# Kernel tuning notes

Hardware: AMD Instinct MI355X
Metric: run time of the kernel (lower is better)

## Reference

```python
import jax, jax.numpy as jnp
from jax import lax
import numpy as np

B, T, H, E = 4096, 16, 1024, 1024


def setup_inputs() -> dict:
    key = jax.random.key(0)
    ks = jax.random.split(key, 6)
    query = jax.random.normal(ks[0], (B, H), dtype=jnp.float32)
    topics = jax.random.normal(ks[1], (B, T, E), dtype=jnp.float32)
    coverage_vector = jax.random.uniform(ks[2], (B, T), dtype=jnp.float32)
    # Ua: Linear(embed->hidden, bias=False); weight [H, E]
    Ua_w = jax.random.normal(ks[3], (H, E), dtype=jnp.float32) * 0.03
    # Wa: Linear(hidden->hidden, bias=False). Applied repeatedly (T times) to
    # query in the original loop, so keep spectral norm < 1 for stability.
    Wa_w = jax.random.normal(ks[4], (H, H), dtype=jnp.float32) * 0.01
    # va: Linear(hidden->1, bias=True)
    va_w = jax.random.normal(ks[5], (1, H), dtype=jnp.float32) * 0.03
    va_b = jnp.zeros((1,), dtype=jnp.float32)
    return {"query": query, "topics": topics, "coverage_vector": coverage_vector,
            "Ua_w": Ua_w, "Wa_w": Wa_w, "va_w": va_w, "va_b": va_b}


def reference(query, topics, coverage_vector, Ua_w, Wa_w, va_w, va_b):
    # proj_key for all steps at once: Ua(topics[:, i, :]) -> [B, T, H]
    proj_keys = jnp.einsum('bte,he->bth', topics, Ua_w)
    # Original loop mutates query = Wa(query) each step, so step i uses
    # Wa^(i+1) @ query. Sequential dependence -> lax.scan over T.
    def step(q, pk_c):
        pk, c = pk_c                       # pk: [B, H], c: [B]
        q = q @ Wa_w.T                     # query = Wa(query)
        s = (jnp.tanh(q + pk) @ va_w.T)[:, 0] + va_b[0]  # va(tanh(.)) -> [B]
        return q, s * c                    # scale by coverage C_t[:, i]
    xs = (jnp.swapaxes(proj_keys, 0, 1), coverage_vector.T)  # [T,B,H], [T,B]
    _, scores = lax.scan(step, query, xs)  # scores: [T, B]
    scores = scores.T                      # [B, T]
    alphas = jax.nn.softmax(scores, axis=1)
    mt = jnp.einsum('bt,bte->be', alphas, topics)  # bmm(alphas[:,None,:], topics)
    return mt, alphas
```

## Files before the change

### kernel.cpp

```cpp
#include <hip/hip_runtime.h>

typedef unsigned short u16;
typedef unsigned int u32;
typedef __attribute__((ext_vector_type(8))) __bf16 bf16x8;
typedef __attribute__((ext_vector_type(4))) float f32x4;

__device__ __forceinline__ u16 f2bf(float f) {
  u32 u = __float_as_uint(f);
  u32 r = (u + 0x7FFFu + ((u >> 16) & 1u)) >> 16;
  return (u16)r;
}

__device__ __forceinline__ void gload_lds16(const void* g, void* l) {
  __builtin_amdgcn_global_load_lds((const __attribute__((address_space(1))) u32*)g,
                                   (__attribute__((address_space(3))) u32*)l, 16, 0, 0);
}

__device__ __forceinline__ float fast_tanh(float x) {
  x = fminf(fmaxf(x, -15.f), 15.f);
  float e2 = __expf(2.f * x);
  return (e2 - 1.f) / (e2 + 1.f);
}

__global__ __launch_bounds__(256) void cvt_kernel(const float* __restrict__ src,
                                                  u16* __restrict__ dst, int n4) {
  int stride = gridDim.x * blockDim.x;
  for (int i = blockIdx.x * blockDim.x + threadIdx.x; i < n4; i += stride) {
    float4 v = reinterpret_cast<const float4*>(src)[i];
    ushort4 o;
    o.x = f2bf(v.x); o.y = f2bf(v.y); o.z = f2bf(v.z); o.w = f2bf(v.w);
    reinterpret_cast<ushort4*>(dst)[i] = o;
  }
}

__global__ __launch_bounds__(256) void cvt3_kernel(const float* __restrict__ q_src, u16* __restrict__ q_dst,
                                                   const float* __restrict__ u_src, u16* __restrict__ u_dst,
                                                   const float* __restrict__ w_src, u16* __restrict__ w_dst) {
  int b = blockIdx.x;
  const float* src; u16* dst; int i;
  if (b < 4096)      { src = q_src; dst = q_dst; i = b * 256 + threadIdx.x; }
  else if (b < 5120) { src = u_src; dst = u_dst; i = (b - 4096) * 256 + threadIdx.x; }
  else               { src = w_src; dst = w_dst; i = (b - 5120) * 256 + threadIdx.x; }
  float4 v = reinterpret_cast<const float4*>(src)[i];
  ushort4 o;
  o.x = f2bf(v.x); o.y = f2bf(v.y); o.z = f2bf(v.z); o.w = f2bf(v.w);
  reinterpret_cast<ushort4*>(dst)[i] = o;
}

__global__ __launch_bounds__(256) void transpose_bf16_kernel(const float* __restrict__ src,
                                                             u16* __restrict__ dst) {
  __shared__ float tile[32][33];
  int tx = threadIdx.x & 31, ty = threadIdx.x >> 5;
  int bx = blockIdx.x * 32, by = blockIdx.y * 32;
#pragma unroll
  for (int j = 0; j < 32; j += 8)
    tile[ty + j][tx] = src[(size_t)(by + ty + j) * 1024 + bx + tx];
  __syncthreads();
#pragma unroll
  for (int j = 0; j < 32; j += 8)
    dst[(size_t)(bx + ty + j) * 1024 + by + tx] = f2bf(tile[tx][ty + j]);
}

__device__ __forceinline__ void stage_tile(const u16* __restrict__ g, size_t row_stride,
                                           u16* lds, int tid) {
#pragma unroll
  for (int s = 0; s < 4; ++s) {
    int chunk = s * 256 + tid;
    int row = chunk >> 3;
    int kcl = (chunk & 7) ^ (row & 7);
    const u16* gp = g + (size_t)row * row_stride + (size_t)(kcl * 8);
    u16* lp = lds + (tid >> 6) * 512 + s * 2048;
    gload_lds16(gp, lp);
  }
}

struct PowArgs {
  const u16* A[8];
  const u16* Bt[8];
  u16* C[8];
  u16* Ct[8];
};

__global__ __launch_bounds__(256) void pow_gemm_kernel(PowArgs args) {
  const u16* A  = args.A[blockIdx.z];
  const u16* Bt = args.Bt[blockIdx.z];
  u16* C  = args.C[blockIdx.z];
  u16* Ct = args.Ct[blockIdx.z];

  __shared__ __align__(16) u16 As[8192];
  __shared__ __align__(16) u16 Bs[8192];

  int tid = threadIdx.x;
  int lane = tid & 63, wave = tid >> 6;
  int wr = wave >> 1, wc = wave & 1;
  int lr = lane & 15, lg = lane >> 4;
  int m0 = blockIdx.x * 128, n0 = blockIdx.y * 128;

  f32x4 acc[4][4];
  const f32x4 zero = {0.f, 0.f, 0.f, 0.f};
#pragma unroll
  for (int m = 0; m < 4; ++m)
#pragma unroll
    for (int n = 0; n < 4; ++n) acc[m][n] = zero;

  for (int k0 = 0; k0 < 1024; k0 += 64) {
    stage_tile(A + (size_t)m0 * 1024 + k0, 1024, As, tid);
    stage_tile(Bt + (size_t)n0 * 1024 + k0, 1024, Bs, tid);
    __syncthreads();
#pragma unroll
    for (int ks = 0; ks < 2; ++ks) {
      bf16x8 a[4], b[4];
#pragma unroll
      for (int m = 0; m < 4; ++m) {
        int ra = wr * 64 + m * 16 + lr;
        a[m] = *reinterpret_cast<const bf16x8*>(As + ra * 64 + (((ks * 4 + lg) ^ (ra & 7)) << 3));
      }
#pragma unroll
      for (int n = 0; n < 4; ++n) {
        int rb = wc * 64 + n * 16 + lr;
        b[n] = *reinterpret_cast<const bf16x8*>(Bs + rb * 64 + (((ks * 4 + lg) ^ (rb & 7)) << 3));
      }
#pragma unroll
      for (int m = 0; m < 4; ++m)
#pragma unroll
        for (int n = 0; n < 4; ++n)
          acc[m][n] = __builtin_amdgcn_mfma_f32_16x16x32_bf16(a[m], b[n], acc[m][n], 0, 0, 0);
    }
    __syncthreads();
  }

#pragma unroll
  for (int m = 0; m < 4; ++m) {
    int row0 = m0 + wr * 64 + m * 16 + lg * 4;
#pragma unroll
    for (int n = 0; n < 4; ++n) {
      int col = n0 + wc * 64 + n * 16 + lr;
      f32x4 c = acc[m][n];
      ushort4 pk;
      pk.x = f2bf(c[0]); pk.y = f2bf(c[1]); pk.z = f2bf(c[2]); pk.w = f2bf(c[3]);
      C[(size_t)(row0 + 0) * 1024 + col] = pk.x;
      C[(size_t)(row0 + 1) * 1024 + col] = pk.y;
      C[(size_t)(row0 + 2) * 1024 + col] = pk.z;
      C[(size_t)(row0 + 3) * 1024 + col] = pk.w;
      *reinterpret_cast<ushort4*>(Ct + (size_t)col * 1024 + row0) = pk;
    }
  }
}


#define PHASE_READS(CUR, KS, MH)                                                 \
  { _Pragma("unroll") for (int i_ = 0; i_ < 4; ++i_) af[i_] = lda(CUR, KS, (MH)*4 + i_); \
    if ((MH) == 0) { _Pragma("unroll") for (int n_ = 0; n_ < 4; ++n_) bfr[n_] = ldb(CUR, KS, n_); } }

#define PHASE_MFMA(MH)                                                           \
  { __builtin_amdgcn_s_barrier();                                                \
    asm volatile("s_waitcnt lgkmcnt(0)" ::: "memory");                           \
    __builtin_amdgcn_sched_barrier(0);                                           \
    __builtin_amdgcn_s_setprio(1);                                               \
    _Pragma("unroll") for (int i_ = 0; i_ < 4; ++i_)                             \
      _Pragma("unroll") for (int n_ = 0; n_ < 4; ++n_)                           \
        acc[(MH)*4 + i_][n_] =                                                   \
            __builtin_amdgcn_mfma_f32_16x16x32_bf16(af[i_], bfr[n_], acc[(MH)*4 + i_][n_], 0, 0, 0); \
    __builtin_amdgcn_s_setprio(0); }

#define PHASE_END()                                                              \
  { __builtin_amdgcn_s_barrier(); __builtin_amdgcn_sched_barrier(0); }

__global__ __launch_bounds__(512, 2) void score8_kernel(
    const u16* __restrict__ query_bf, const u16* __restrict__ topics_bf,
    const u16* __restrict__ F_base, const u16* __restrict__ Ua_bf,
    const float* __restrict__ va_w, float* __restrict__ scores_raw) {
  extern __shared__ __align__(16) char lds[];

  const int tid = threadIdx.x;
  const int lane = tid & 63, wave = tid >> 6;
  const int wm = wave >> 2, wn = wave & 3;
  const int lr = lane & 15, lg = lane >> 4;
  const int m0 = blockIdx.x * 256, n0 = blockIdx.y * 256;
  const int t = blockIdx.z;
  const int NT = 32;

  const u16* Ft = F_base + (size_t)t * (1024 * 1024);

  auto a_src = [&](int kt, const u16*& p, int& str) {
    if (kt < 16) { p = query_bf + (size_t)m0 * 1024 + kt * 64; str = 1024; }
    else { p = topics_bf + (size_t)m0 * 16384 + (size_t)t * 1024 + (kt - 16) * 64; str = 16384; }
  };
  auto b_src = [&](int kt, const u16*& p, int& str) {
    if (kt < 16) { p = Ft + (size_t)n0 * 1024 + kt * 64; str = 1024; }
    else { p = Ua_bf + (size_t)n0 * 1024 + (kt - 16) * 64; str = 1024; }
  };

  auto stage = [&](const u16* p, int str, int ks, int lds_byte) {
#pragma unroll
    for (int s = 0; s < 2; ++s) {
      int c = s * 512 + tid;
      int row = c >> 2;
      int cl = (c & 3) ^ ((row >> 1) & 3);
      const u16* gp = p + (size_t)row * str + ks * 32 + cl * 8;
      char* lp = lds + lds_byte + s * 8192 + (tid >> 6) * 1024;
      gload_lds16(gp, lp);
    }
  };

  auto lda = [&](int cur, int ks, int m) -> bf16x8 {
    int row = wm * 128 + m * 16 + lr;
    int byte = cur * 65536 + ks * 16384 + row * 64 + ((lg ^ ((row >> 1) & 3)) << 4);
    return *reinterpret_cast<const bf16x8*>(lds + byte);
  };
  auto ldb = [&](int cur, int ks, int n) -> bf16x8 {
    int row = wn * 64 + n * 16 + lr;
    int byte = cur * 65536 + 32768 + ks * 16384 + row * 64 + ((lg ^ ((row >> 1) & 3)) << 4);
    return *reinterpret_cast<const bf16x8*>(lds + byte);
  };

  f32x4 acc[8][4];
  const f32x4 zero = {0.f, 0.f, 0.f, 0.f};
#pragma unroll
  for (int m = 0; m < 8; ++m)
#pragma unroll
    for (int n = 0; n < 4; ++n) acc[m][n] = zero;

  bf16x8 af[4], bfr[4];
  const u16 *ap, *bp; int as_, bs_;

  a_src(0, ap, as_); stage(ap, as_, 0, 0);
  b_src(0, bp, bs_); stage(bp, bs_, 0, 32768);
  a_src(0, ap, as_); stage(ap, as_, 1, 16384);
  b_src(0, bp, bs_); stage(bp, bs_, 1, 49152);
  a_src(1, ap, as_); stage(ap, as_, 0, 65536);
  b_src(1, bp, bs_); stage(bp, bs_, 0, 65536 + 32768);
  asm volatile("s_waitcnt vmcnt(4)" ::: "memory");
  __builtin_amdgcn_s_barrier();
  __builtin_amdgcn_sched_barrier(0);

#pragma unroll 2
  for (int kt = 0; kt < NT; ++kt) {
    int cur = kt & 1, nxt = cur ^ 1;
    PHASE_READS(cur, 0, 0);
    if (kt + 1 < NT) { a_src(kt + 1, ap, as_); stage(ap, as_, 1, nxt * 65536 + 16384); }
    PHASE_MFMA(0); PHASE_END();
    PHASE_READS(cur, 0, 1);
    if (kt + 1 < NT) { b_src(kt + 1, bp, bs_); stage(bp, bs_, 1, nxt * 65536 + 49152); }
    PHASE_MFMA(1); PHASE_END();
    PHASE_READS(cur, 1, 0);
    if (kt + 2 < NT) { a_src(kt + 2, ap, as_); stage(ap, as_, 0, cur * 65536); }
    PHASE_MFMA(0); PHASE_END();
    PHASE_READS(cur, 1, 1);
    if (kt + 2 < NT) { b_src(kt + 2, bp, bs_); stage(bp, bs_, 0, cur * 65536 + 32768); }
    PHASE_MFMA(1);
    if (kt < NT - 2)       { asm volatile("s_waitcnt vmcnt(4)" ::: "memory"); }
    else if (kt == NT - 2) { asm volatile("s_waitcnt vmcnt(0)" ::: "memory"); }
    PHASE_END();
  }

  float va_c[4];
#pragma unroll
  for (int n = 0; n < 4; ++n) va_c[n] = va_w[n0 + wn * 64 + n * 16 + lr];

  float* sred = (float*)lds;
#pragma unroll
  for (int m = 0; m < 8; ++m) {
    float rs[4] = {0.f, 0.f, 0.f, 0.f};
#pragma unroll
    for (int n = 0; n < 4; ++n) {
      f32x4 c = acc[m][n];
      rs[0] += va_c[n] * fast_tanh(c[0]);
      rs[1] += va_c[n] * fast_tanh(c[1]);
      rs[2] += va_c[n] * fast_tanh(c[2]);
      rs[3] += va_c[n] * fast_tanh(c[3]);
    }
#pragma unroll
    for (int j = 0; j < 4; ++j) {
      float v = rs[j];
      v += __shfl_xor(v, 1);
      v += __shfl_xor(v, 2);
      v += __shfl_xor(v, 4);
      v += __shfl_xor(v, 8);
      if (lr == 0) sred[wn * 256 + wm * 128 + m * 16 + lg * 4 + j] = v;
    }
  }
  __syncthreads();
  if (tid < 256) {
    float s = sred[tid] + sred[256 + tid] + sred[512 + tid] + sred[768 + tid];
    atomicAdd(&scores_raw[(size_t)(m0 + tid) * 16 + t], s);
  }
}

__global__ __launch_bounds__(256) void softmax_mt_kernel(
    const float* __restrict__ scores_raw, const float* __restrict__ cov,
    const float* __restrict__ topics, const float* __restrict__ va_b,
    float* __restrict__ mt, float* __restrict__ alphas) {
  int b = blockIdx.x;
  int tid = threadIdx.x;
  float vb = va_b[0];
  float e[16];
  float mx = -3.4e38f;
#pragma unroll
  for (int t = 0; t < 16; ++t) {
    float s = (scores_raw[b * 16 + t] + vb) * cov[b * 16 + t];
    e[t] = s;
    mx = fmaxf(mx, s);
  }
  float sum = 0.f;
#pragma unroll
  for (int t = 0; t < 16; ++t) { e[t] = __expf(e[t] - mx); sum += e[t]; }
  float inv = 1.f / sum;
  if (tid == 0) {
#pragma unroll
    for (int t = 0; t < 16; ++t) alphas[b * 16 + t] = e[t] * inv;
  }
  const float4* tp = reinterpret_cast<const float4*>(topics + (size_t)b * 16384);
  float4 accv = {0.f, 0.f, 0.f, 0.f};
#pragma unroll
  for (int t = 0; t < 16; ++t) {
    float4 v = tp[t * 256 + tid];
    float a = e[t] * inv;
    accv.x += a * v.x; accv.y += a * v.y; accv.z += a * v.z; accv.w += a * v.w;
  }
  reinterpret_cast<float4*>(mt + (size_t)b * 1024)[tid] = accv;
}

extern "C" void kernel_launch(void* const* d_in, const int* in_sizes, int n_in,
                              void* d_out, int out_size, void* d_ws, size_t ws_size,
                              hipStream_t stream) {
  (void)in_sizes; (void)n_in; (void)out_size; (void)ws_size;
  const float* query = (const float*)d_in[0];
  const float* topics = (const float*)d_in[1];
  const float* cov   = (const float*)d_in[2];
  const float* Ua    = (const float*)d_in[3];
  const float* Wa    = (const float*)d_in[4];
  const float* va_w  = (const float*)d_in[5];
  const float* va_b  = (const float*)d_in[6];

  float* mt = (float*)d_out;
  float* alphas = mt + (size_t)4096 * 1024;

  char* ws = (char*)d_ws;
  u16* topics_bf = (u16*)(ws);
  u16* query_bf  = (u16*)(ws + (size_t)128 * 1024 * 1024);
  u16* Ua_bf     = (u16*)(ws + (size_t)136 * 1024 * 1024);
  u16* F_base    = (u16*)(ws + (size_t)138 * 1024 * 1024);
  u16* FT_base   = (u16*)(ws + (size_t)170 * 1024 * 1024);
  float* scores_raw = (float*)(ws + (size_t)202 * 1024 * 1024);

  hipFuncSetAttribute(reinterpret_cast<const void*>(score8_kernel),
                      hipFuncAttributeMaxDynamicSharedMemorySize, 131072);

  hipMemsetAsync(scores_raw, 0, (size_t)4096 * 16 * sizeof(float), stream);

  cvt_kernel<<<8192, 256, 0, stream>>>(topics, topics_bf, 16777216);
  cvt3_kernel<<<6144, 256, 0, stream>>>(query, query_bf, Ua, Ua_bf, Wa, F_base);
  transpose_bf16_kernel<<<dim3(32, 32), 256, 0, stream>>>(Wa, FT_base);

  const size_t MS = 1024 * 1024;
  auto F  = [&](int i) { return F_base + (size_t)i * MS; };
  auto FT = [&](int i) { return FT_base + (size_t)i * MS; };

  PowArgs a1{};
  a1.A[0] = F(0); a1.Bt[0] = FT(0); a1.C[0] = F(1); a1.Ct[0] = FT(1);
  pow_gemm_kernel<<<dim3(8, 8, 1), 256, 0, stream>>>(a1);
  PowArgs a2{};
  a2.A[0] = F(1); a2.Bt[0] = FT(0); a2.C[0] = F(2); a2.Ct[0] = FT(2);
  a2.A[1] = F(1); a2.Bt[1] = FT(1); a2.C[1] = F(3); a2.Ct[1] = FT(3);
  pow_gemm_kernel<<<dim3(8, 8, 2), 256, 0, stream>>>(a2);
  PowArgs a3{};
  for (int p = 0; p < 4; ++p) { a3.A[p] = F(3); a3.Bt[p] = FT(p); a3.C[p] = F(4 + p); a3.Ct[p] = FT(4 + p); }
  pow_gemm_kernel<<<dim3(8, 8, 4), 256, 0, stream>>>(a3);
  PowArgs a4{};
  for (int p = 0; p < 8; ++p) { a4.A[p] = F(7); a4.Bt[p] = FT(p); a4.C[p] = F(8 + p); a4.Ct[p] = FT(8 + p); }
  pow_gemm_kernel<<<dim3(8, 8, 8), 256, 0, stream>>>(a4);

  score8_kernel<<<dim3(16, 4, 16), 512, 131072, stream>>>(query_bf, topics_bf, F_base, Ua_bf,
                                                          va_w, scores_raw);
  softmax_mt_kernel<<<4096, 256, 0, stream>>>(scores_raw, cov, topics, va_b, mt, alphas);
}
```

Before: 823.0 us.

## Use 64x64-tile GEMM for early Wa powers and precompute score kernel offsets

Adds a smaller-tile pow64_gemm kernel for the first two Wa power stages, which had too few 128x128 blocks to fill the GPU. It also rearranges the score kernel's LDS layout into separate A/B regions and precomputes per-lane LDS and global offsets, removing per-iteration address arithmetic and branchy source selection. The small-tile kernel has no double buffering and gets less reuse, and the precomputed offsets add register pressure.

```diff
diff --git a/kernel.cpp b/kernel.cpp
--- a/kernel.cpp
+++ b/kernel.cpp
@@ -147,23 +147,105 @@
   }
 }
 
-
-#define PHASE_READS(CUR, KS, MH)                                                 \
-  { _Pragma("unroll") for (int i_ = 0; i_ < 4; ++i_) af[i_] = lda(CUR, KS, (MH)*4 + i_); \
-    if ((MH) == 0) { _Pragma("unroll") for (int n_ = 0; n_ < 4; ++n_) bfr[n_] = ldb(CUR, KS, n_); } }
-
-#define PHASE_MFMA(MH)                                                           \
-  { __builtin_amdgcn_s_barrier();                                                \
-    asm volatile("s_waitcnt lgkmcnt(0)" ::: "memory");                           \
-    __builtin_amdgcn_sched_barrier(0);                                           \
-    __builtin_amdgcn_s_setprio(1);                                               \
-    _Pragma("unroll") for (int i_ = 0; i_ < 4; ++i_)                             \
-      _Pragma("unroll") for (int n_ = 0; n_ < 4; ++n_)                           \
-        acc[(MH)*4 + i_][n_] =                                                   \
+__device__ __forceinline__ void stage_tile64(const u16* __restrict__ g, u16* lds, int tid) {
+#pragma unroll
+  for (int s = 0; s < 2; ++s) {
+    int chunk = s * 256 + tid;
+    int row = chunk >> 3;
+    int kcl = (chunk & 7) ^ (row & 7);
+    const u16* gp = g + (size_t)row * 1024 + (size_t)(kcl * 8);
+    u16* lp = lds + (tid >> 6) * 512 + s * 2048;
+    gload_lds16(gp, lp);
+  }
+}
+
+__global__ __launch_bounds__(256) void pow64_gemm_kernel(PowArgs args) {
+  const u16* A  = args.A[blockIdx.z];
+  const u16* Bt = args.Bt[blockIdx.z];
+  u16* C  = args.C[blockIdx.z];
+  u16* Ct = args.Ct[blockIdx.z];
+
+  __shared__ __align__(16) u16 As[4096];
+  __shared__ __align__(16) u16 Bs[4096];
+
+  int tid = threadIdx.x;
+  int lane = tid & 63, wave = tid >> 6;
+  int wr = wave >> 1, wc = wave & 1;
+  int lr = lane & 15, lg = lane >> 4;
+  int m0 = blockIdx.x * 64, n0 = blockIdx.y * 64;
+
+  f32x4 acc[2][2];
+  const f32x4 zero = {0.f, 0.f, 0.f, 0.f};
+#pragma unroll
+  for (int m = 0; m < 2; ++m)
+#pragma unroll
+    for (int n = 0; n < 2; ++n) acc[m][n] = zero;
+
+  for (int k0 = 0; k0 < 1024; k0 += 64) {
+    stage_tile64(A + (size_t)m0 * 1024 + k0, As, tid);
+    stage_tile64(Bt + (size_t)n0 * 1024 + k0, Bs, tid);
+    __syncthreads();
+#pragma unroll
+    for (int ks = 0; ks < 2; ++ks) {
+      bf16x8 a[2], b[2];
+#pragma unroll
+      for (int m = 0; m < 2; ++m) {
+        int ra = wr * 32 + m * 16 + lr;
+        a[m] = *reinterpret_cast<const bf16x8*>(As + ra * 64 + (((ks * 4 + lg) ^ (ra & 7)) << 3));
+      }
+#pragma unroll
+      for (int n = 0; n < 2; ++n) {
+        int rb = wc * 32 + n * 16 + lr;
+        b[n] = *reinterpret_cast<const bf16x8*>(Bs + rb * 64 + (((ks * 4 + lg) ^ (rb & 7)) << 3));
+      }
+#pragma unroll
+      for (int m = 0; m < 2; ++m)
+#pragma unroll
+        for (int n = 0; n < 2; ++n)
+          acc[m][n] = __builtin_amdgcn_mfma_f32_16x16x32_bf16(a[m], b[n], acc[m][n], 0, 0, 0);
+    }
+    __syncthreads();
+  }
+
+#pragma unroll
+  for (int m = 0; m < 2; ++m) {
+    int row0 = m0 + wr * 32 + m * 16 + lg * 4;
+#pragma unroll
+    for (int n = 0; n < 2; ++n) {
+      int col = n0 + wc * 32 + n * 16 + lr;
+      f32x4 c = acc[m][n];
+      ushort4 pk;
+      pk.x = f2bf(c[0]); pk.y = f2bf(c[1]); pk.z = f2bf(c[2]); pk.w = f2bf(c[3]);
+      C[(size_t)(row0 + 0) * 1024 + col] = pk.x;
+      C[(size_t)(row0 + 1) * 1024 + col] = pk.y;
+      C[(size_t)(row0 + 2) * 1024 + col] = pk.z;
+      C[(size_t)(row0 + 3) * 1024 + col] = pk.w;
+      *reinterpret_cast<ushort4*>(Ct + (size_t)col * 1024 + row0) = pk;
+    }
+  }
+}
+
+
+#define PHASE_READS(CUR, KS, MH)                                                     \
+  { _Pragma("unroll") for (int i_ = 0; i_ < 4; ++i_)                                 \
+      af[i_] = *reinterpret_cast<const bf16x8*>(lds + aoffv[(MH)*4 + i_] +           \
+                                                (CUR)*32768 + (KS)*16384);           \
+    if ((MH) == 0) { _Pragma("unroll") for (int n_ = 0; n_ < 4; ++n_)                \
+      bfr[n_] = *reinterpret_cast<const bf16x8*>(lds + boffv[n_] +                   \
+                                                 (CUR)*32768 + (KS)*16384); } }
+
+#define PHASE_MFMA(MH)                                                               \
+  { __builtin_amdgcn_s_barrier();                                                    \
+    asm volatile("s_waitcnt lgkmcnt(0)" ::: "memory");                               \
+    __builtin_amdgcn_sched_barrier(0);                                               \
+    __builtin_amdgcn_s_setprio(1);                                                   \
+    _Pragma("unroll") for (int i_ = 0; i_ < 4; ++i_)                                 \
+      _Pragma("unroll") for (int n_ = 0; n_ < 4; ++n_)                               \
+        acc[(MH)*4 + i_][n_] =                                                       \
             __builtin_amdgcn_mfma_f32_16x16x32_bf16(af[i_], bfr[n_], acc[(MH)*4 + i_][n_], 0, 0, 0); \
     __builtin_amdgcn_s_setprio(0); }
 
-#define PHASE_END()                                                              \
+#define PHASE_END()                                                                  \
   { __builtin_amdgcn_s_barrier(); __builtin_amdgcn_sched_barrier(0); }
 
 __global__ __launch_bounds__(512, 2) void score8_kernel(
@@ -182,36 +264,46 @@
 
   const u16* Ft = F_base + (size_t)t * (1024 * 1024);
 
-  auto a_src = [&](int kt, const u16*& p, int& str) {
-    if (kt < 16) { p = query_bf + (size_t)m0 * 1024 + kt * 64; str = 1024; }
-    else { p = topics_bf + (size_t)m0 * 16384 + (size_t)t * 1024 + (kt - 16) * 64; str = 16384; }
+  u32 aoffv[8], boffv[4];
+#pragma unroll
+  for (int m = 0; m < 8; ++m) {
+    int row = wm * 128 + m * 16 + lr;
+    aoffv[m] = row * 64 + ((lg ^ ((row >> 1) & 3)) << 4);
+  }
+#pragma unroll
+  for (int n = 0; n < 4; ++n) {
+    int row = wn * 64 + n * 16 + lr;
+    boffv[n] = 65536 + row * 64 + ((lg ^ ((row >> 1) & 3)) << 4);
+  }
+
+  u32 goff1[2], goff2[2];
+#pragma unroll
+  for (int s = 0; s < 2; ++s) {
+    int c = s * 512 + tid;
+    int row = c >> 2;
+    int cl = (c & 3) ^ ((row >> 1) & 3);
+    goff1[s] = row * 1024 + cl * 8;
+    goff2[s] = row * 16384 + cl * 8;
+  }
+  char* sdst = lds + (tid >> 6) * 1024;
+  const u16* qbase = query_bf + (size_t)m0 * 1024;
+  const u16* tbase = topics_bf + (size_t)m0 * 16384 + (size_t)t * 1024 - 1024;
+  const u16* fbase = Ft + (size_t)n0 * 1024;
+  const u16* ubase = Ua_bf + (size_t)n0 * 1024 - 1024;
+
+  auto stageA = [&](int kt, int ks, int buf) {
+    const u16* base = (kt < 16 ? qbase : tbase) + kt * 64 + ks * 32;
+#pragma unroll
+    for (int s = 0; s < 2; ++s) {
+      u32 off = (kt < 16) ? goff1[s] : goff2[s];
+      gload_lds16(base + off, sdst + buf * 32768 + ks * 16384 + s * 8192);
+    }
   };
-  auto b_src = [&](int kt, const u16*& p, int& str) {
-    if (kt < 16) { p = Ft + (size_t)n0 * 1024 + kt * 64; str = 1024; }
-    else { p = Ua_bf + (size_t)n0 * 1024 + (kt - 16) * 64; str = 1024; }
-  };
-
-  auto stage = [&](const u16* p, int str, int ks, int lds_byte) {
-#pragma unroll
-    for (int s = 0; s < 2; ++s) {
-      int c = s * 512 + tid;
-      int row = c >> 2;
-      int cl = (c & 3) ^ ((row >> 1) & 3);
-      const u16* gp = p + (size_t)row * str + ks * 32 + cl * 8;
-      char* lp = lds + lds_byte + s * 8192 + (tid >> 6) * 1024;
-      gload_lds16(gp, lp);
-    }
-  };
-
-  auto lda = [&](int cur, int ks, int m) -> bf16x8 {
-    int row = wm * 128 + m * 16 + lr;
-    int byte = cur * 65536 + ks * 16384 + row * 64 + ((lg ^ ((row >> 1) & 3)) << 4);
-    return *reinterpret_cast<const bf16x8*>(lds + byte);
-  };
-  auto ldb = [&](int cur, int ks, int n) -> bf16x8 {
-    int row = wn * 64 + n * 16 + lr;
-    int byte = cur * 65536 + 32768 + ks * 16384 + row * 64 + ((lg ^ ((row >> 1) & 3)) << 4);
-    return *reinterpret_cast<const bf16x8*>(lds + byte);
+  auto stageB = [&](int kt, int ks, int buf) {
+    const u16* base = (kt < 16 ? fbase : ubase) + kt * 64 + ks * 32;
+#pragma unroll
+    for (int s = 0; s < 2; ++s)
+      gload_lds16(base + goff1[s], sdst + 65536 + buf * 32768 + ks * 16384 + s * 8192);
   };
 
   f32x4 acc[8][4];
@@ -222,14 +314,10 @@
     for (int n = 0; n < 4; ++n) acc[m][n] = zero;
 
   bf16x8 af[4], bfr[4];
-  const u16 *ap, *bp; int as_, bs_;
-
-  a_src(0, ap, as_); stage(ap, as_, 0, 0);
-  b_src(0, bp, bs_); stage(bp, bs_, 0, 32768);
-  a_src(0, ap, as_); stage(ap, as_, 1, 16384);
-  b_src(0, bp, bs_); stage(bp, bs_, 1, 49152);
-  a_src(1, ap, as_); stage(ap, as_, 0, 65536);
-  b_src(1, bp, bs_); stage(bp, bs_, 0, 65536 + 32768);
+
+  stageA(0, 0, 0); stageB(0, 0, 0);
+  stageA(0, 1, 0); stageB(0, 1, 0);
+  stageA(1, 0, 1); stageB(1, 0, 1);
   asm volatile("s_waitcnt vmcnt(4)" ::: "memory");
   __builtin_amdgcn_s_barrier();
   __builtin_amdgcn_sched_barrier(0);
@@ -238,16 +326,16 @@
   for (int kt = 0; kt < NT; ++kt) {
     int cur = kt & 1, nxt = cur ^ 1;
     PHASE_READS(cur, 0, 0);
-    if (kt + 1 < NT) { a_src(kt + 1, ap, as_); stage(ap, as_, 1, nxt * 65536 + 16384); }
+    if (kt + 1 < NT) stageA(kt + 1, 1, nxt);
     PHASE_MFMA(0); PHASE_END();
     PHASE_READS(cur, 0, 1);
-    if (kt + 1 < NT) { b_src(kt + 1, bp, bs_); stage(bp, bs_, 1, nxt * 65536 + 49152); }
+    if (kt + 1 < NT) stageB(kt + 1, 1, nxt);
     PHASE_MFMA(1); PHASE_END();
     PHASE_READS(cur, 1, 0);
-    if (kt + 2 < NT) { a_src(kt + 2, ap, as_); stage(ap, as_, 0, cur * 65536); }
+    if (kt + 2 < NT) stageA(kt + 2, 0, cur);
     PHASE_MFMA(0); PHASE_END();
     PHASE_READS(cur, 1, 1);
-    if (kt + 2 < NT) { b_src(kt + 2, bp, bs_); stage(bp, bs_, 0, cur * 65536 + 32768); }
+    if (kt + 2 < NT) stageB(kt + 2, 0, cur);
     PHASE_MFMA(1);
     if (kt < NT - 2)       { asm volatile("s_waitcnt vmcnt(4)" ::: "memory"); }
     else if (kt == NT - 2) { asm volatile("s_waitcnt vmcnt(0)" ::: "memory"); }
@@ -359,11 +447,11 @@
 
   PowArgs a1{};
   a1.A[0] = F(0); a1.Bt[0] = FT(0); a1.C[0] = F(1); a1.Ct[0] = FT(1);
-  pow_gemm_kernel<<<dim3(8, 8, 1), 256, 0, stream>>>(a1);
+  pow64_gemm_kernel<<<dim3(16, 16, 1), 256, 0, stream>>>(a1);
   PowArgs a2{};
   a2.A[0] = F(1); a2.Bt[0] = FT(0); a2.C[0] = F(2); a2.Ct[0] = FT(2);
   a2.A[1] = F(1); a2.Bt[1] = FT(1); a2.C[1] = F(3); a2.Ct[1] = FT(3);
-  pow_gemm_kernel<<<dim3(8, 8, 2), 256, 0, stream>>>(a2);
+  pow64_gemm_kernel<<<dim3(16, 16, 2), 256, 0, stream>>>(a2);
   PowArgs a3{};
   for (int p = 0; p < 4; ++p) { a3.A[p] = F(3); a3.Bt[p] = FT(p); a3.C[p] = F(4 + p); a3.Ct[p] = FT(4 + p); }
   pow_gemm_kernel<<<dim3(8, 8, 4), 256, 0, stream>>>(a3);
```

New measurement: 817.8 us. About the same (-0.6%).
